# Performance work log

Hardware: AMD Instinct MI355X
Metric: run time of the kernel (lower is better)

The kernel has to match this reference:

```python
import jax, jax.numpy as jnp
import numpy as np

T, N, E = 24, 50000, 800000
IN_F, HID, OUT_F, K = 11, 128, 3, 2


def setup_inputs() -> dict:
    key = jax.random.key(0)
    ks = jax.random.split(key, 8)
    X_seq = jax.random.normal(ks[0], (T, N, IN_F), jnp.float32)
    # monotone time channel (col 6) so dt = X[t+1][:,6] - X[t][:,6] > 0 in the rollout
    times = 0.1 * jnp.arange(T, dtype=jnp.float32)
    X_seq = X_seq.at[:, :, 6].set(jnp.broadcast_to(times[:, None], (T, N)))
    edge_index = jax.random.randint(ks[1], (2, E), 0, N, dtype=jnp.int32)
    s = 0.1
    Wx = s * jax.random.normal(ks[2], (3, K, IN_F, HID), jnp.float32)
    bx = s * jax.random.normal(ks[3], (3, HID), jnp.float32)
    Wh = s * jax.random.normal(ks[4], (3, K, HID, HID), jnp.float32)
    bh = s * jax.random.normal(ks[5], (3, HID), jnp.float32)
    W_head = s * jax.random.normal(ks[6], (HID, OUT_F), jnp.float32)
    b_head = s * jax.random.normal(ks[7], (OUT_F,), jnp.float32)
    return {"X_seq": X_seq, "edge_index": edge_index, "Wx": Wx, "bx": bx,
            "Wh": Wh, "bh": bh, "W_head": W_head, "b_head": b_head}


def reference(X_seq, edge_index, Wx, bx, Wh, bh, W_head, b_head):
    n = X_seq.shape[1]
    src, dst = edge_index[0], edge_index[1]
    # PyG ChebConv sym-normalized scaled Laplacian with lambda_max=2:
    # L_hat = -D^{-1/2} A D^{-1/2}  (zero diagonal)
    deg = jax.ops.segment_sum(jnp.ones(src.shape[0], X_seq.dtype), src, num_segments=n)
    dinv = jnp.where(deg > 0, 1.0 / jnp.sqrt(deg), 0.0)
    w = -(dinv[src] * dinv[dst])  # [E]

    def lap(x):  # x: [N, F] -> L_hat @ x via gather/scatter over edges
        return jax.ops.segment_sum(w[:, None] * x[src], dst, num_segments=n)

    def cheb(x, W, b):  # K=2 ChebConv: Tx0 @ W0 + (L_hat x) @ W1 + bias
        return x @ W[0] + lap(x) @ W[1] + b

    def gru(x, h):  # GConvGRU cell
        z = jax.nn.sigmoid(cheb(x, Wx[0], bx[0]) + cheb(h, Wh[0], bh[0]))
        r = jax.nn.sigmoid(cheb(x, Wx[1], bx[1]) + cheb(h, Wh[1], bh[1]))
        h_tilde = jnp.tanh(cheb(x, Wx[2], bx[2]) + cheb(h * r, Wh[2], bh[2]))
        return z * h + (1.0 - z) * h_tilde

    hid = W_head.shape[0]
    h0 = gru(X_seq[0], jnp.zeros((n, hid), X_seq.dtype))
    u0 = h0 @ W_head + b_head  # [N, 3]
    dt = X_seq[1:, :, 6] - X_seq[:-1, :, 6]  # [T-1, N]

    def step(carry, inp):
        h, u_prev, prev_pos = carry
        x_orig, dt_t = inp
        pos = jax.lax.stop_gradient(u_prev)        # next_u = u.detach()
        vel = (pos - prev_pos) / dt_t[:, None]     # X[t+1][:,8:11]
        x = jnp.concatenate([x_orig[:, :3], pos, x_orig[:, 6:8], vel], axis=1)
        h = gru(x, h)
        u = h @ W_head + b_head
        return (h, u, pos), u

    _, outs = jax.lax.scan(step, (h0, u0, X_seq[0, :, 3:6]), (X_seq[1:], dt))
    return jnp.concatenate([u0[None], outs], axis=0)  # [T, N, 3]
```

## Files before the change

### kernel.cpp

```cpp
#include <hip/hip_runtime.h>
#include <hip/hip_bf16.h>
#include <math.h>

#define NN 50000
#define EE 800000
#define TT 24
#define HID 128

static constexpr int KTOT = 288;

typedef __attribute__((ext_vector_type(8))) short v8s;
typedef __attribute__((ext_vector_type(4))) float v4f;

__device__ __forceinline__ float fast_sigmoid(float v) {
    float e = __expf(-v);
    return __builtin_amdgcn_rcpf(1.0f + e);
}
__device__ __forceinline__ float fast_tanh(float v) {
    float e2 = __expf(2.0f * v);
    return 1.0f - 2.0f * __builtin_amdgcn_rcpf(e2 + 1.0f);
}

__device__ __forceinline__ unsigned short f2bf(float v) {
    __hip_bfloat16 b = __float2bfloat16(v);
    return *reinterpret_cast<unsigned short*>(&b);
}
__device__ __forceinline__ float bf2f(unsigned short u) {
    __hip_bfloat16 b = *reinterpret_cast<__hip_bfloat16*>(&u);
    return __bfloat162float(b);
}
__device__ __forceinline__ void split3(float v, unsigned short& u0, unsigned short& u1, unsigned short& u2) {
    u0 = f2bf(v);  float r1 = v - bf2f(u0);
    u1 = f2bf(r1); float r2 = r1 - bf2f(u1);
    u2 = f2bf(r2);
}


__global__ void count_deg_kernel(const int* __restrict__ src, const int* __restrict__ dst,
                                 int* __restrict__ deg_src, int* __restrict__ cnt_dst) {
    int e = blockIdx.x * blockDim.x + threadIdx.x;
    if (e < EE) {
        atomicAdd(&deg_src[src[e]], 1);
        atomicAdd(&cnt_dst[dst[e]], 1);
    }
}

__global__ void dinv_kernel(const int* __restrict__ deg, float* __restrict__ dinv) {
    int i = blockIdx.x * blockDim.x + threadIdx.x;
    if (i < NN) {
        int d = deg[i];
        dinv[i] = (d > 0) ? 1.0f / sqrtf((float)d) : 0.0f;
    }
}

__global__ void scan_kernel(const int* __restrict__ cnt, int* __restrict__ row_ptr) {
    __shared__ int buf[2][1024];
    __shared__ int carry_s;
    int tid = threadIdx.x;
    if (tid == 0) carry_s = 0;
    __syncthreads();
    for (int base = 0; base < NN; base += 1024) {
        int i = base + tid;
        int v = (i < NN) ? cnt[i] : 0;
        int pb = 0;
        buf[0][tid] = v;
        __syncthreads();
        for (int off = 1; off < 1024; off <<= 1) {
            int t = buf[pb][tid] + ((tid >= off) ? buf[pb][tid - off] : 0);
            buf[pb ^ 1][tid] = t;
            pb ^= 1;
            __syncthreads();
        }
        int incl = buf[pb][tid];
        int carry = carry_s;
        if (i < NN) row_ptr[i] = carry + incl - v;
        __syncthreads();
        if (tid == 0) carry_s = carry + buf[pb][1023];
        __syncthreads();
    }
    if (tid == 0) row_ptr[NN] = carry_s;
}

__global__ void fill_csr_kernel(const int* __restrict__ src, const int* __restrict__ dst,
                                const int* __restrict__ row_ptr, int* __restrict__ fillp,
                                const float* __restrict__ dinv,
                                int2* __restrict__ csr) {
    int e = blockIdx.x * blockDim.x + threadIdx.x;
    if (e < EE) {
        int s = src[e], d = dst[e];
        int p = row_ptr[d] + atomicAdd(&fillp[d], 1);
        float w = -(dinv[s] * dinv[d]);
        csr[p] = make_int2(s, __float_as_int(w));
    }
}

__global__ void pack_weights_kernel(const float* __restrict__ Wx, const float* __restrict__ bx,
                                    const float* __restrict__ Wh, const float* __restrict__ bh,
                                    unsigned short* __restrict__ WA0, unsigned short* __restrict__ WA1,
                                    unsigned short* __restrict__ WA2,
                                    unsigned short* __restrict__ WB0, unsigned short* __restrict__ WB1,
                                    unsigned short* __restrict__ WB2,
                                    float* __restrict__ biasA, float* __restrict__ biasB) {
    const int NAW = 256 * KTOT, NBW = 128 * KTOT;
    int idx = blockIdx.x * blockDim.x + threadIdx.x;
    if (idx < NAW) {
        int j = idx / KTOT, k = idx % KTOT;
        int g = j >> 7, jj = j & 127;
        float v;
        if (k < 16)       v = (k < 11) ? Wx[((g*2 + 0)*11 + k) * 128 + jj] : 0.0f;
        else if (k < 32)  { int kk = k - 16; v = (kk < 11) ? Wx[((g*2 + 1)*11 + kk) * 128 + jj] : 0.0f; }
        else if (k < 160) v = Wh[((g*2 + 0)*128 + (k - 32)) * 128 + jj];
        else              v = Wh[((g*2 + 1)*128 + (k - 160)) * 128 + jj];
        unsigned short u0, u1, u2; split3(v, u0, u1, u2);
        WA0[idx] = u0; WA1[idx] = u1; WA2[idx] = u2;
    } else if (idx < NAW + NBW) {
        int t = idx - NAW;
        int j = t / KTOT, k = t % KTOT;
        int jj = j;
        float v;
        if (k < 16)       v = (k < 11) ? Wx[(4*11 + k) * 128 + jj] : 0.0f;
        else if (k < 32)  { int kk = k - 16; v = (kk < 11) ? Wx[(5*11 + kk) * 128 + jj] : 0.0f; }
        else if (k < 160) v = Wh[(4*128 + (k - 32)) * 128 + jj];
        else              v = Wh[(5*128 + (k - 160)) * 128 + jj];
        unsigned short u0, u1, u2; split3(v, u0, u1, u2);
        WB0[t] = u0; WB1[t] = u1; WB2[t] = u2;
    } else if (idx < NAW + NBW + 256) {
        int j = idx - (NAW + NBW);
        int g = j >> 7, jj = j & 127;
        biasA[j] = bx[g*128 + jj] + bh[g*128 + jj];
    } else if (idx < NAW + NBW + 256 + 128) {
        int jj = idx - (NAW + NBW + 256);
        biasB[jj] = bx[2*128 + jj] + bh[2*128 + jj];
    }
}


__global__ void copy_x0_kernel(const float* __restrict__ Xin, float* __restrict__ xbuf,
                               unsigned short* __restrict__ X0p, unsigned short* __restrict__ X1p,
                               unsigned short* __restrict__ X2p) {
    int i = blockIdx.x * blockDim.x + threadIdx.x;
    if (i >= NN) return;
    float vals[16];
    #pragma unroll
    for (int c = 0; c < 11; c++) vals[c] = Xin[(size_t)i*11 + c];
    #pragma unroll
    for (int c = 11; c < 16; c++) vals[c] = 0.0f;
    #pragma unroll
    for (int c = 0; c < 16; c++) {
        xbuf[(size_t)i*16 + c] = vals[c];
        unsigned short u0, u1, u2; split3(vals[c], u0, u1, u2);
        X0p[(size_t)i*32 + c] = u0; X1p[(size_t)i*32 + c] = u1; X2p[(size_t)i*32 + c] = u2;
    }
}

__global__ void build_x_kernel(const float* __restrict__ Xt, const float* __restrict__ Xtm1,
                               const float* __restrict__ pos, const float* __restrict__ prevbase,
                               int prev_stride, int prev_off,
                               float* __restrict__ xbuf,
                               unsigned short* __restrict__ X0p, unsigned short* __restrict__ X1p,
                               unsigned short* __restrict__ X2p) {
    int i = blockIdx.x * blockDim.x + threadIdx.x;
    if (i >= NN) return;
    const float* xo = Xt + (size_t)i * 11;
    float tnow  = xo[6];
    float tprev = Xtm1[(size_t)i * 11 + 6];
    float inv = 1.0f / (tnow - tprev);
    float p0 = pos[(size_t)i*3 + 0], p1 = pos[(size_t)i*3 + 1], p2 = pos[(size_t)i*3 + 2];
    const float* pp = prevbase + (size_t)i * prev_stride + prev_off;
    float vals[16];
    vals[0] = xo[0]; vals[1] = xo[1]; vals[2] = xo[2];
    vals[3] = p0;    vals[4] = p1;    vals[5] = p2;
    vals[6] = tnow;  vals[7] = xo[7];
    vals[8] = (p0 - pp[0]) * inv; vals[9] = (p1 - pp[1]) * inv; vals[10] = (p2 - pp[2]) * inv;
    vals[11] = vals[12] = vals[13] = vals[14] = vals[15] = 0.0f;
    #pragma unroll
    for (int c = 0; c < 16; c++) {
        xbuf[(size_t)i*16 + c] = vals[c];
        unsigned short u0, u1, u2; split3(vals[c], u0, u1, u2);
        X0p[(size_t)i*32 + c] = u0; X1p[(size_t)i*32 + c] = u1; X2p[(size_t)i*32 + c] = u2;
    }
}

__global__ void lap_small_kernel(const int* __restrict__ row_ptr, const int2* __restrict__ csr,
                                 const float* __restrict__ xbuf,
                                 unsigned short* __restrict__ X0p, unsigned short* __restrict__ X1p,
                                 unsigned short* __restrict__ X2p) {
    int node = blockIdx.x * 16 + (threadIdx.x >> 4);
    int f = threadIdx.x & 15;
    if (node >= NN) return;
    int b = row_ptr[node], e = row_ptr[node + 1];
    float acc = 0.0f;
    for (int p = b; p < e; p++) {
        int2 ed = csr[p];
        acc += __int_as_float(ed.y) * xbuf[(size_t)ed.x*16 + f];
    }
    unsigned short u0, u1, u2; split3(acc, u0, u1, u2);
    X0p[(size_t)node*32 + 16 + f] = u0;
    X1p[(size_t)node*32 + 16 + f] = u1;
    X2p[(size_t)node*32 + 16 + f] = u2;
}

__global__ __launch_bounds__(256)
void lap_big_kernel(const int* __restrict__ row_ptr, const int2* __restrict__ csr,
                    const float* __restrict__ hin,
                    unsigned short* __restrict__ H0p, unsigned short* __restrict__ H1p,
                    unsigned short* __restrict__ H2p) {
    int tid  = threadIdx.x;
    int node = blockIdx.x * 4 + (tid >> 6);
    if (node >= NN) return;
    int eo = (tid >> 5) & 1;
    int f  = tid & 31;
    const float4* h4 = (const float4*)hin;
    float4 acc0 = make_float4(0.f, 0.f, 0.f, 0.f);
    float4 acc1 = make_float4(0.f, 0.f, 0.f, 0.f);
    int b = row_ptr[node], e = row_ptr[node + 1];
    int p = b;
    for (; p + 3 < e; p += 4) {
        int2 ea = csr[p + eo];
        int2 eb = csr[p + 2 + eo];
        float wa = __int_as_float(ea.y);
        float wb = __int_as_float(eb.y);
        float4 va = h4[(size_t)ea.x*32 + f];
        float4 vb = h4[(size_t)eb.x*32 + f];
        acc0.x += wa * va.x; acc0.y += wa * va.y; acc0.z += wa * va.z; acc0.w += wa * va.w;
        acc1.x += wb * vb.x; acc1.y += wb * vb.y; acc1.z += wb * vb.z; acc1.w += wb * vb.w;
    }
    for (; p + 1 < e; p += 2) {
        int2 ea = csr[p + eo];
        float wa = __int_as_float(ea.y);
        float4 va = h4[(size_t)ea.x*32 + f];
        acc0.x += wa * va.x; acc0.y += wa * va.y; acc0.z += wa * va.z; acc0.w += wa * va.w;
    }
    if (p < e && eo == 0) {
        int2 ea = csr[p];
        float wa = __int_as_float(ea.y);
        float4 va = h4[(size_t)ea.x*32 + f];
        acc0.x += wa * va.x; acc0.y += wa * va.y; acc0.z += wa * va.z; acc0.w += wa * va.w;
    }
    acc0.x += acc1.x; acc0.y += acc1.y; acc0.z += acc1.z; acc0.w += acc1.w;
    acc0.x += __shfl_xor(acc0.x, 32);
    acc0.y += __shfl_xor(acc0.y, 32);
    acc0.z += __shfl_xor(acc0.z, 32);
    acc0.w += __shfl_xor(acc0.w, 32);
    if (eo == 0) {
        size_t base = (size_t)node*256 + 128 + f*4;
        float a[4] = {acc0.x, acc0.y, acc0.z, acc0.w};
        ushort4 s0, s1, s2;
        unsigned short u0, u1, u2;
        split3(a[0], u0, u1, u2); s0.x = u0; s1.x = u1; s2.x = u2;
        split3(a[1], u0, u1, u2); s0.y = u0; s1.y = u1; s2.y = u2;
        split3(a[2], u0, u1, u2); s0.z = u0; s1.z = u1; s2.z = u2;
        split3(a[3], u0, u1, u2); s0.w = u0; s1.w = u1; s2.w = u2;
        *(ushort4*)(H0p + base) = s0;
        *(ushort4*)(H1p + base) = s1;
        *(ushort4*)(H2p + base) = s2;
    }
}

template<int NOUT, int EPI>
__global__ __launch_bounds__(256)
void gemm_mfma_kernel(const unsigned short* __restrict__ X0p, const unsigned short* __restrict__ X1p,
                      const unsigned short* __restrict__ X2p,
                      const unsigned short* __restrict__ H0p, const unsigned short* __restrict__ H1p,
                      const unsigned short* __restrict__ H2p,
                      const unsigned short* __restrict__ W0, const unsigned short* __restrict__ W1,
                      const unsigned short* __restrict__ W2,
                      const float* __restrict__ bias,
                      float* __restrict__ p0, float* __restrict__ p1, const float* __restrict__ p2,
                      unsigned short* __restrict__ S0, unsigned short* __restrict__ S1,
                      unsigned short* __restrict__ S2)
{
    const int tid  = threadIdx.x;
    const int lane = tid & 63, wid = tid >> 6;
    const int l15 = lane & 15, chunk = lane >> 4;
    const int row0 = blockIdx.x * 64 + (wid >> 1) * 32;
    const int col0 = blockIdx.y * 64 + (wid & 1) * 32;
    int ar0 = row0 + l15;      if (ar0 >= NN) ar0 = NN - 1;
    int ar1 = row0 + 16 + l15; if (ar1 >= NN) ar1 = NN - 1;
    const int bc0 = col0 + l15, bc1 = col0 + 16 + l15;

    v4f acc[2][2];
    v4f z4 = {0.f, 0.f, 0.f, 0.f};
    acc[0][0] = z4; acc[0][1] = z4; acc[1][0] = z4; acc[1][1] = z4;

    v8s a0[2], a1[2], a2[2], b0[2], b1[2], b2[2];

    {
        size_t oa0 = (size_t)ar0*32 + chunk*8, oa1 = (size_t)ar1*32 + chunk*8;
        size_t ob0 = (size_t)bc0*KTOT + chunk*8, ob1 = (size_t)bc1*KTOT + chunk*8;
        a0[0] = *(const v8s*)(X0p + oa0); a1[0] = *(const v8s*)(X1p + oa0); a2[0] = *(const v8s*)(X2p + oa0);
        a0[1] = *(const v8s*)(X0p + oa1); a1[1] = *(const v8s*)(X1p + oa1); a2[1] = *(const v8s*)(X2p + oa1);
        b0[0] = *(const v8s*)(W0 + ob0);  b1[0] = *(const v8s*)(W1 + ob0);  b2[0] = *(const v8s*)(W2 + ob0);
        b0[1] = *(const v8s*)(W0 + ob1);  b1[1] = *(const v8s*)(W1 + ob1);  b2[1] = *(const v8s*)(W2 + ob1);
        #pragma unroll
        for (int mi = 0; mi < 2; mi++)
            #pragma unroll
            for (int ni = 0; ni < 2; ni++) {
                v4f c = acc[mi][ni];
                c = __builtin_amdgcn_mfma_f32_16x16x32_bf16(a0[mi], b0[ni], c, 0, 0, 0);
                c = __builtin_amdgcn_mfma_f32_16x16x32_bf16(a0[mi], b1[ni], c, 0, 0, 0);
                c = __builtin_amdgcn_mfma_f32_16x16x32_bf16(a1[mi], b0[ni], c, 0, 0, 0);
                c = __builtin_amdgcn_mfma_f32_16x16x32_bf16(a0[mi], b2[ni], c, 0, 0, 0);
                c = __builtin_amdgcn_mfma_f32_16x16x32_bf16(a1[mi], b1[ni], c, 0, 0, 0);
                c = __builtin_amdgcn_mfma_f32_16x16x32_bf16(a2[mi], b0[ni], c, 0, 0, 0);
                acc[mi][ni] = c;
            }
    }
    #pragma unroll
    for (int ks = 1; ks < 9; ks++) {
        int ka = (ks - 1) * 32 + chunk * 8;
        int kb = ks * 32 + chunk * 8;
        size_t oa0 = (size_t)ar0*256 + ka, oa1 = (size_t)ar1*256 + ka;
        size_t ob0 = (size_t)bc0*KTOT + kb, ob1 = (size_t)bc1*KTOT + kb;
        a0[0] = *(const v8s*)(H0p + oa0); a1[0] = *(const v8s*)(H1p + oa0); a2[0] = *(const v8s*)(H2p + oa0);
        a0[1] = *(const v8s*)(H0p + oa1); a1[1] = *(const v8s*)(H1p + oa1); a2[1] = *(const v8s*)(H2p + oa1);
        b0[0] = *(const v8s*)(W0 + ob0);  b1[0] = *(const v8s*)(W1 + ob0);  b2[0] = *(const v8s*)(W2 + ob0);
        b0[1] = *(const v8s*)(W0 + ob1);  b1[1] = *(const v8s*)(W1 + ob1);  b2[1] = *(const v8s*)(W2 + ob1);
        #pragma unroll
        for (int mi = 0; mi < 2; mi++)
            #pragma unroll
            for (int ni = 0; ni < 2; ni++) {
                v4f c = acc[mi][ni];
                c = __builtin_amdgcn_mfma_f32_16x16x32_bf16(a0[mi], b0[ni], c, 0, 0, 0);
                c = __builtin_amdgcn_mfma_f32_16x16x32_bf16(a0[mi], b1[ni], c, 0, 0, 0);
                c = __builtin_amdgcn_mfma_f32_16x16x32_bf16(a1[mi], b0[ni], c, 0, 0, 0);
                c = __builtin_amdgcn_mfma_f32_16x16x32_bf16(a0[mi], b2[ni], c, 0, 0, 0);
                c = __builtin_amdgcn_mfma_f32_16x16x32_bf16(a1[mi], b1[ni], c, 0, 0, 0);
                c = __builtin_amdgcn_mfma_f32_16x16x32_bf16(a2[mi], b0[ni], c, 0, 0, 0);
                acc[mi][ni] = c;
            }
    }

    #pragma unroll
    for (int mi = 0; mi < 2; mi++)
        #pragma unroll
        for (int ni = 0; ni < 2; ni++) {
            int cc = col0 + ni*16 + l15;
            float bv = bias[cc];
            #pragma unroll
            for (int r = 0; r < 4; r++) {
                int row = row0 + mi*16 + chunk*4 + r;
                if (row >= NN) continue;
                float v = acc[mi][ni][r] + bv;
                if (EPI == 0) {
                    float s = fast_sigmoid(v);
                    if (cc < HID) {
                        p0[(size_t)row*HID + cc] = s;
                    } else {
                        int c = cc - HID;
                        float hr = p2[(size_t)row*HID + c] * s;
                        p1[(size_t)row*HID + c] = hr;
                        unsigned short u0, u1, u2; split3(hr, u0, u1, u2);
                        S0[(size_t)row*256 + c] = u0;
                        S1[(size_t)row*256 + c] = u1;
                        S2[(size_t)row*256 + c] = u2;
                    }
                } else {
                    float ht = fast_tanh(v);
                    float zz   = p0[(size_t)row*HID + cc];
                    float hold = p1[(size_t)row*HID + cc];
                    float hn = zz*hold + (1.0f - zz)*ht;
                    p1[(size_t)row*HID + cc] = hn;
                    unsigned short u0, u1, u2; split3(hn, u0, u1, u2);
                    S0[(size_t)row*256 + cc] = u0;
                    S1[(size_t)row*256 + cc] = u1;
                    S2[(size_t)row*256 + cc] = u2;
                }
            }
        }
}

__global__ void head_kernel(const float* __restrict__ h, const float* __restrict__ Whead,
                            const float* __restrict__ bhead, float* __restrict__ out) {
    int node = blockIdx.x * 4 + (threadIdx.x >> 6);
    int lane = threadIdx.x & 63;
    if (node >= NN) return;
    float h0 = h[(size_t)node*128 + lane];
    float h1 = h[(size_t)node*128 + 64 + lane];
    float p[3];
    #pragma unroll
    for (int j = 0; j < 3; j++)
        p[j] = h0 * Whead[lane*3 + j] + h1 * Whead[(64 + lane)*3 + j];
    #pragma unroll
    for (int off = 32; off > 0; off >>= 1) {
        p[0] += __shfl_down(p[0], off);
        p[1] += __shfl_down(p[1], off);
        p[2] += __shfl_down(p[2], off);
    }
    if (lane == 0) {
        out[(size_t)node*3 + 0] = p[0] + bhead[0];
        out[(size_t)node*3 + 1] = p[1] + bhead[1];
        out[(size_t)node*3 + 2] = p[2] + bhead[2];
    }
}


extern "C" void kernel_launch(void* const* d_in, const int* in_sizes, int n_in,
                              void* d_out, int out_size, void* d_ws, size_t ws_size,
                              hipStream_t stream) {
    const float* X_seq  = (const float*)d_in[0];
    const int*   eidx   = (const int*)  d_in[1];
    const float* Wx     = (const float*)d_in[2];
    const float* bx     = (const float*)d_in[3];
    const float* Wh     = (const float*)d_in[4];
    const float* bh     = (const float*)d_in[5];
    const float* Whead  = (const float*)d_in[6];
    const float* bhead  = (const float*)d_in[7];
    float* out = (float*)d_out;

    const int* src = eidx;
    const int* dst = eidx + EE;

    char* base = (char*)d_ws;
    size_t off = 0;
    auto carve = [&](size_t bytes) -> void* {
        void* p = base + off;
        off += (bytes + 255) & ~(size_t)255;
        return p;
    };
    int*   deg_i   = (int*)  carve((size_t)NN * 4);
    int*   cnt     = (int*)  carve((size_t)NN * 4);
    int*   fillp   = (int*)  carve((size_t)NN * 4);
    int*   row_ptr = (int*)  carve((size_t)(NN + 1) * 4);
    float* dinv    = (float*)carve((size_t)NN * 4);
    int2*  csr     = (int2*) carve((size_t)EE * 8);
    unsigned short* WA0 = (unsigned short*)carve((size_t)256 * KTOT * 2);
    unsigned short* WA1 = (unsigned short*)carve((size_t)256 * KTOT * 2);
    unsigned short* WA2 = (unsigned short*)carve((size_t)256 * KTOT * 2);
    unsigned short* WB0 = (unsigned short*)carve((size_t)128 * KTOT * 2);
    unsigned short* WB1 = (unsigned short*)carve((size_t)128 * KTOT * 2);
    unsigned short* WB2 = (unsigned short*)carve((size_t)128 * KTOT * 2);
    float* biasA   = (float*)carve(256 * 4);
    float* biasB   = (float*)carve(128 * 4);
    float* xbuf    = (float*)carve((size_t)NN * 16 * 4);
    unsigned short* X0p = (unsigned short*)carve((size_t)NN * 32 * 2);
    unsigned short* X1p = (unsigned short*)carve((size_t)NN * 32 * 2);
    unsigned short* X2p = (unsigned short*)carve((size_t)NN * 32 * 2);
    float* hbuf    = (float*)carve((size_t)NN * 128 * 4);
    unsigned short* HA0 = (unsigned short*)carve((size_t)NN * 256 * 2);
    unsigned short* HA1 = (unsigned short*)carve((size_t)NN * 256 * 2);
    unsigned short* HA2 = (unsigned short*)carve((size_t)NN * 256 * 2);
    float* hrbuf   = (float*)carve((size_t)NN * 128 * 4);
    unsigned short* HB0 = (unsigned short*)carve((size_t)NN * 256 * 2);
    unsigned short* HB1 = (unsigned short*)carve((size_t)NN * 256 * 2);
    unsigned short* HB2 = (unsigned short*)carve((size_t)NN * 256 * 2);
    float* zbuf    = (float*)carve((size_t)NN * 128 * 4);
    (void)ws_size; (void)n_in; (void)in_sizes; (void)out_size;

    hipMemsetAsync(deg_i, 0, (size_t)NN * 4, stream);
    hipMemsetAsync(cnt,   0, (size_t)NN * 4, stream);
    hipMemsetAsync(fillp, 0, (size_t)NN * 4, stream);
    hipMemsetAsync(hbuf,  0, (size_t)NN * 128 * 4, stream);
    hipMemsetAsync(HA0,   0, (size_t)NN * 256 * 2, stream);
    hipMemsetAsync(HA1,   0, (size_t)NN * 256 * 2, stream);
    hipMemsetAsync(HA2,   0, (size_t)NN * 256 * 2, stream);

    count_deg_kernel<<<(EE + 255) / 256, 256, 0, stream>>>(src, dst, deg_i, cnt);
    dinv_kernel<<<(NN + 255) / 256, 256, 0, stream>>>(deg_i, dinv);
    scan_kernel<<<1, 1024, 0, stream>>>(cnt, row_ptr);
    fill_csr_kernel<<<(EE + 255) / 256, 256, 0, stream>>>(src, dst, row_ptr, fillp, dinv, csr);
    {
        int total = 256*KTOT + 128*KTOT + 256 + 128;
        pack_weights_kernel<<<(total + 255) / 256, 256, 0, stream>>>(Wx, bx, Wh, bh,
            WA0, WA1, WA2, WB0, WB1, WB2, biasA, biasB);
    }

    const int gridN256 = (NN + 255) / 256;
    const int gridM = (NN + 63) / 64;
    const dim3 gridGA(gridM, 4);
    const dim3 gridGB(gridM, 2);

    for (int t = 0; t < TT; t++) {
        if (t == 0) {
            copy_x0_kernel<<<gridN256, 256, 0, stream>>>(X_seq, xbuf, X0p, X1p, X2p);
        } else {
            const float* Xt   = X_seq + (size_t)t * NN * 11;
            const float* Xtm1 = X_seq + (size_t)(t - 1) * NN * 11;
            const float* pos  = out + (size_t)(t - 1) * NN * 3;
            const float* prevbase;
            int pstride, poff;
            if (t == 1) { prevbase = X_seq; pstride = 11; poff = 3; }
            else        { prevbase = out + (size_t)(t - 2) * NN * 3; pstride = 3; poff = 0; }
            build_x_kernel<<<gridN256, 256, 0, stream>>>(Xt, Xtm1, pos, prevbase, pstride, poff,
                                                         xbuf, X0p, X1p, X2p);
        }

        lap_small_kernel<<<(NN + 15) / 16, 256, 0, stream>>>(row_ptr, csr, xbuf, X0p, X1p, X2p);
        lap_big_kernel<<<(NN + 3) / 4, 256, 0, stream>>>(row_ptr, csr, hbuf, HA0, HA1, HA2);

        gemm_mfma_kernel<256, 0><<<gridGA, 256, 0, stream>>>(X0p, X1p, X2p, HA0, HA1, HA2,
                                                             WA0, WA1, WA2, biasA,
                                                             zbuf, hrbuf, hbuf, HB0, HB1, HB2);
        lap_big_kernel<<<(NN + 3) / 4, 256, 0, stream>>>(row_ptr, csr, hrbuf, HB0, HB1, HB2);

        gemm_mfma_kernel<128, 1><<<gridGB, 256, 0, stream>>>(X0p, X1p, X2p, HB0, HB1, HB2,
                                                             WB0, WB1, WB2, biasB,
                                                             zbuf, hbuf, nullptr, HA0, HA1, HA2);

        head_kernel<<<(NN + 3) / 4, 256, 0, stream>>>(hbuf, Whead, bhead, out + (size_t)t * NN * 3);
    }
}
```

Baseline: 9.185 ms.

## Retile MFMA GEMM so each block covers all output columns for 64 rows

Each wave now computes a 64x64 output tile (4x4 MFMA sub-tiles) and a block spans every output column for its 64 rows, replacing the 2D grid of 64x64 block tiles. The A operands (three bf16 split planes of the activations) are loaded once per block row instead of once per column block, which cuts redundant global reads of the large activation matrices. The cost is a much larger accumulator set per wave (64 floats plus operands), which raises register pressure and lowers occupancy, and fewer blocks are launched. The second GEMM now launches 128 threads to match its 128 output columns.

```diff
diff --git a/kernel.cpp b/kernel.cpp
--- a/kernel.cpp
+++ b/kernel.cpp
@@ -273,69 +273,62 @@
     const int tid  = threadIdx.x;
     const int lane = tid & 63, wid = tid >> 6;
     const int l15 = lane & 15, chunk = lane >> 4;
-    const int row0 = blockIdx.x * 64 + (wid >> 1) * 32;
-    const int col0 = blockIdx.y * 64 + (wid & 1) * 32;
-    int ar0 = row0 + l15;      if (ar0 >= NN) ar0 = NN - 1;
-    int ar1 = row0 + 16 + l15; if (ar1 >= NN) ar1 = NN - 1;
-    const int bc0 = col0 + l15, bc1 = col0 + 16 + l15;
-
-    v4f acc[2][2];
+    const int row0 = blockIdx.x * 64;
+    const int wcol0 = wid * 64;
+
+    int ar[4];
+    #pragma unroll
+    for (int mi = 0; mi < 4; mi++) {
+        int r = row0 + mi*16 + l15;
+        ar[mi] = (r < NN) ? r : NN - 1;
+    }
+
+    v4f acc[4][4];
     v4f z4 = {0.f, 0.f, 0.f, 0.f};
-    acc[0][0] = z4; acc[0][1] = z4; acc[1][0] = z4; acc[1][1] = z4;
-
-    v8s a0[2], a1[2], a2[2], b0[2], b1[2], b2[2];
-
-    {
-        size_t oa0 = (size_t)ar0*32 + chunk*8, oa1 = (size_t)ar1*32 + chunk*8;
-        size_t ob0 = (size_t)bc0*KTOT + chunk*8, ob1 = (size_t)bc1*KTOT + chunk*8;
-        a0[0] = *(const v8s*)(X0p + oa0); a1[0] = *(const v8s*)(X1p + oa0); a2[0] = *(const v8s*)(X2p + oa0);
-        a0[1] = *(const v8s*)(X0p + oa1); a1[1] = *(const v8s*)(X1p + oa1); a2[1] = *(const v8s*)(X2p + oa1);
-        b0[0] = *(const v8s*)(W0 + ob0);  b1[0] = *(const v8s*)(W1 + ob0);  b2[0] = *(const v8s*)(W2 + ob0);
-        b0[1] = *(const v8s*)(W0 + ob1);  b1[1] = *(const v8s*)(W1 + ob1);  b2[1] = *(const v8s*)(W2 + ob1);
+    #pragma unroll
+    for (int mi = 0; mi < 4; mi++)
         #pragma unroll
-        for (int mi = 0; mi < 2; mi++)
+        for (int ni = 0; ni < 4; ni++) acc[mi][ni] = z4;
+
+    #pragma unroll
+    for (int ks = 0; ks < 9; ks++) {
+        v8s a0[4], a1[4], a2[4];
+        #pragma unroll
+        for (int mi = 0; mi < 4; mi++) {
+            size_t oa = (ks == 0) ? ((size_t)ar[mi]*32 + chunk*8)
+                                  : ((size_t)ar[mi]*256 + (ks-1)*32 + chunk*8);
+            const unsigned short* P0 = (ks == 0) ? X0p : H0p;
+            const unsigned short* P1 = (ks == 0) ? X1p : H1p;
+            const unsigned short* P2 = (ks == 0) ? X2p : H2p;
+            a0[mi] = *(const v8s*)(P0 + oa);
+            a1[mi] = *(const v8s*)(P1 + oa);
+            a2[mi] = *(const v8s*)(P2 + oa);
+        }
+        #pragma unroll
+        for (int ni = 0; ni < 4; ni++) {
+            size_t ob = (size_t)(wcol0 + ni*16 + l15)*KTOT + ks*32 + chunk*8;
+            v8s b0 = *(const v8s*)(W0 + ob);
+            v8s b1 = *(const v8s*)(W1 + ob);
+            v8s b2 = *(const v8s*)(W2 + ob);
             #pragma unroll
-            for (int ni = 0; ni < 2; ni++) {
+            for (int mi = 0; mi < 4; mi++) {
                 v4f c = acc[mi][ni];
-                c = __builtin_amdgcn_mfma_f32_16x16x32_bf16(a0[mi], b0[ni], c, 0, 0, 0);
-                c = __builtin_amdgcn_mfma_f32_16x16x32_bf16(a0[mi], b1[ni], c, 0, 0, 0);
-                c = __builtin_amdgcn_mfma_f32_16x16x32_bf16(a1[mi], b0[ni], c, 0, 0, 0);
-                c = __builtin_amdgcn_mfma_f32_16x16x32_bf16(a0[mi], b2[ni], c, 0, 0, 0);
-                c = __builtin_amdgcn_mfma_f32_16x16x32_bf16(a1[mi], b1[ni], c, 0, 0, 0);
-                c = __builtin_amdgcn_mfma_f32_16x16x32_bf16(a2[mi], b0[ni], c, 0, 0, 0);
+                c = __builtin_amdgcn_mfma_f32_16x16x32_bf16(a0[mi], b0, c, 0, 0, 0);
+                c = __builtin_amdgcn_mfma_f32_16x16x32_bf16(a0[mi], b1, c, 0, 0, 0);
+                c = __builtin_amdgcn_mfma_f32_16x16x32_bf16(a1[mi], b0, c, 0, 0, 0);
+                c = __builtin_amdgcn_mfma_f32_16x16x32_bf16(a0[mi], b2, c, 0, 0, 0);
+                c = __builtin_amdgcn_mfma_f32_16x16x32_bf16(a1[mi], b1, c, 0, 0, 0);
+                c = __builtin_amdgcn_mfma_f32_16x16x32_bf16(a2[mi], b0, c, 0, 0, 0);
                 acc[mi][ni] = c;
             }
-    }
-    #pragma unroll
-    for (int ks = 1; ks < 9; ks++) {
-        int ka = (ks - 1) * 32 + chunk * 8;
-        int kb = ks * 32 + chunk * 8;
-        size_t oa0 = (size_t)ar0*256 + ka, oa1 = (size_t)ar1*256 + ka;
-        size_t ob0 = (size_t)bc0*KTOT + kb, ob1 = (size_t)bc1*KTOT + kb;
-        a0[0] = *(const v8s*)(H0p + oa0); a1[0] = *(const v8s*)(H1p + oa0); a2[0] = *(const v8s*)(H2p + oa0);
-        a0[1] = *(const v8s*)(H0p + oa1); a1[1] = *(const v8s*)(H1p + oa1); a2[1] = *(const v8s*)(H2p + oa1);
-        b0[0] = *(const v8s*)(W0 + ob0);  b1[0] = *(const v8s*)(W1 + ob0);  b2[0] = *(const v8s*)(W2 + ob0);
-        b0[1] = *(const v8s*)(W0 + ob1);  b1[1] = *(const v8s*)(W1 + ob1);  b2[1] = *(const v8s*)(W2 + ob1);
+        }
+    }
+
+    #pragma unroll
+    for (int mi = 0; mi < 4; mi++)
         #pragma unroll
-        for (int mi = 0; mi < 2; mi++)
-            #pragma unroll
-            for (int ni = 0; ni < 2; ni++) {
-                v4f c = acc[mi][ni];
-                c = __builtin_amdgcn_mfma_f32_16x16x32_bf16(a0[mi], b0[ni], c, 0, 0, 0);
-                c = __builtin_amdgcn_mfma_f32_16x16x32_bf16(a0[mi], b1[ni], c, 0, 0, 0);
-                c = __builtin_amdgcn_mfma_f32_16x16x32_bf16(a1[mi], b0[ni], c, 0, 0, 0);
-                c = __builtin_amdgcn_mfma_f32_16x16x32_bf16(a0[mi], b2[ni], c, 0, 0, 0);
-                c = __builtin_amdgcn_mfma_f32_16x16x32_bf16(a1[mi], b1[ni], c, 0, 0, 0);
-                c = __builtin_amdgcn_mfma_f32_16x16x32_bf16(a2[mi], b0[ni], c, 0, 0, 0);
-                acc[mi][ni] = c;
-            }
-    }
-
-    #pragma unroll
-    for (int mi = 0; mi < 2; mi++)
-        #pragma unroll
-        for (int ni = 0; ni < 2; ni++) {
-            int cc = col0 + ni*16 + l15;
+        for (int ni = 0; ni < 4; ni++) {
+            int cc = wcol0 + ni*16 + l15;
             float bv = bias[cc];
             #pragma unroll
             for (int r = 0; r < 4; r++) {
@@ -467,8 +460,6 @@
 
     const int gridN256 = (NN + 255) / 256;
     const int gridM = (NN + 63) / 64;
-    const dim3 gridGA(gridM, 4);
-    const dim3 gridGB(gridM, 2);
 
     for (int t = 0; t < TT; t++) {
         if (t == 0) {
@@ -488,14 +479,14 @@
         lap_small_kernel<<<(NN + 15) / 16, 256, 0, stream>>>(row_ptr, csr, xbuf, X0p, X1p, X2p);
         lap_big_kernel<<<(NN + 3) / 4, 256, 0, stream>>>(row_ptr, csr, hbuf, HA0, HA1, HA2);
 
-        gemm_mfma_kernel<256, 0><<<gridGA, 256, 0, stream>>>(X0p, X1p, X2p, HA0, HA1, HA2,
-                                                             WA0, WA1, WA2, biasA,
-                                                             zbuf, hrbuf, hbuf, HB0, HB1, HB2);
+        gemm_mfma_kernel<256, 0><<<gridM, 256, 0, stream>>>(X0p, X1p, X2p, HA0, HA1, HA2,
+                                                            WA0, WA1, WA2, biasA,
+                                                            zbuf, hrbuf, hbuf, HB0, HB1, HB2);
         lap_big_kernel<<<(NN + 3) / 4, 256, 0, stream>>>(row_ptr, csr, hrbuf, HB0, HB1, HB2);
 
-        gemm_mfma_kernel<128, 1><<<gridGB, 256, 0, stream>>>(X0p, X1p, X2p, HB0, HB1, HB2,
-                                                             WB0, WB1, WB2, biasB,
-                                                             zbuf, hbuf, nullptr, HA0, HA1, HA2);
+        gemm_mfma_kernel<128, 1><<<gridM, 128, 0, stream>>>(X0p, X1p, X2p, HB0, HB1, HB2,
+                                                            WB0, WB1, WB2, biasB,
+                                                            zbuf, hbuf, nullptr, HA0, HA1, HA2);
 
         head_kernel<<<(NN + 3) / 4, 256, 0, stream>>>(hbuf, Whead, bhead, out + (size_t)t * NN * 3);
     }
```

Measured after the change: 8.781 ms. 1.05x faster.
